# Performance work log

Measured on AMD Instinct MI355X. Metric: run time of the kernel, lower is better.

## Reference

```python
import jax, jax.numpy as jnp
import numpy as np

B, T, I, H, O = 256, 512, 64, 512, 1


def setup_inputs() -> dict:
    key = jax.random.key(0)
    ks = jax.random.split(key, 8)
    s_ih = 1.0 / np.sqrt(H)
    inp = {
        "x": jax.random.normal(ks[0], (B, T, I), dtype=jnp.float32),
        "W_ih": jax.random.uniform(ks[1], (4 * H, I), minval=-s_ih, maxval=s_ih, dtype=jnp.float32),
        "W_hh": jax.random.uniform(ks[2], (4 * H, H), minval=-s_ih, maxval=s_ih, dtype=jnp.float32),
        "b_ih": jax.random.uniform(ks[3], (4 * H,), minval=-s_ih, maxval=s_ih, dtype=jnp.float32),
        "b_hh": jax.random.uniform(ks[4], (4 * H,), minval=-s_ih, maxval=s_ih, dtype=jnp.float32),
        "W_fc": jax.random.uniform(ks[5], (O, H), minval=-s_ih, maxval=s_ih, dtype=jnp.float32),
        "b_fc": jax.random.uniform(ks[6], (O,), minval=-s_ih, maxval=s_ih, dtype=jnp.float32),
    }
    return inp


def _lstm_last_h(x, W_ih, W_hh, b_ih, b_hh):
    # x: [B, T, I]. Precompute input projection for all timesteps (one big GEMM).
    x_gates = jnp.einsum("bti,gi->btg", x, W_ih) + b_ih + b_hh  # [B, T, 4H]
    x_gates = jnp.swapaxes(x_gates, 0, 1)  # [T, B, 4H] for scan
    hdim = W_hh.shape[1]
    h0 = jnp.zeros((x.shape[0], hdim), dtype=x.dtype)
    c0 = jnp.zeros((x.shape[0], hdim), dtype=x.dtype)

    def step(carry, xg):
        h, c = carry
        gates = xg + h @ W_hh.T  # [B, 4H]
        i, f, g, o = jnp.split(gates, 4, axis=-1)  # PyTorch gate order: i, f, g, o
        i = jax.nn.sigmoid(i)
        f = jax.nn.sigmoid(f)
        g = jnp.tanh(g)
        o = jax.nn.sigmoid(o)
        c = f * c + i * g
        h = o * jnp.tanh(c)
        return (h, c), None

    (h_last, _), _ = jax.lax.scan(step, (h0, c0), x_gates)
    return h_last  # [B, H] == out[:, -1, :] for a single-layer LSTM


def reference(x, W_ih, W_hh, b_ih, b_hh, W_fc, b_fc):
    h_last = _lstm_last_h(x, W_ih, W_hh, b_ih, b_hh)
    return h_last @ W_fc.T + b_fc  # [B, O]
```

## Files before the change

### kernel.cpp

```cpp
#include <hip/hip_runtime.h>

typedef _Float16 h8 __attribute__((ext_vector_type(8)));
typedef float v4f __attribute__((ext_vector_type(4)));

#define B_  256
#define T_  512
#define I_  64
#define H_  512

#define OFF_W16   0
#define OFF_WIH   (OFF_W16 + 2048*512*2)
#define OFF_BIAS  (OFF_WIH + 2048*64*2)
#define OFF_X16   (OFF_BIAS + 2048*4)
#define OFF_H0    (OFF_X16 + 512*256*64*2)
#define OFF_H1    (OFF_H0 + 256*512*2)
#define OFF_CTR   (OFF_H1 + 256*512*2)

__device__ __forceinline__ float sigf(float x) {
    float e = __builtin_amdgcn_exp2f(-1.442695041f * x);
    return __builtin_amdgcn_rcpf(1.f + e);
}
__device__ __forceinline__ float tanhf_(float x) {
    float e = __builtin_amdgcn_exp2f(2.885390082f * x);
    return 1.f - 2.f * __builtin_amdgcn_rcpf(e + 1.f);
}

union Pack4 { _Float16 f[4]; unsigned long long u; };

__global__ void prep_w(const float* __restrict__ Wih, const float* __restrict__ Whh,
                       const float* __restrict__ bih, const float* __restrict__ bhh,
                       _Float16* __restrict__ W16, _Float16* __restrict__ Wih16,
                       float* __restrict__ bias, _Float16* __restrict__ h0,
                       unsigned* __restrict__ ctr) {
    int idx = blockIdx.x * 256 + threadIdx.x;
    W16[idx] = (_Float16)Whh[idx];
    if (idx < 2048 * 64)  Wih16[idx] = (_Float16)Wih[idx];
    if (idx < 2048)       bias[idx] = bih[idx] + bhh[idx];
    if (idx < 32768)
        __hip_atomic_store((unsigned long long*)h0 + idx, 0ull,
                           __ATOMIC_RELAXED, __HIP_MEMORY_SCOPE_AGENT);
    if (idx < 128)
        __hip_atomic_store(ctr + idx, 0u, __ATOMIC_RELAXED, __HIP_MEMORY_SCOPE_AGENT);
}

__global__ void prep_x(const float* __restrict__ x, _Float16* __restrict__ x16) {
    int idx = blockIdx.x * 256 + threadIdx.x;
    int t = idx >> 14;
    int rem = idx & 16383;
    int b = rem >> 6;
    int i = rem & 63;
    x16[idx] = (_Float16)x[((size_t)b * T_ + t) * I_ + i];
}

__launch_bounds__(256, 1)
__global__ void lstm_k(const _Float16* __restrict__ W16, const _Float16* __restrict__ Wih16,
                       const float* __restrict__ bias, const _Float16* __restrict__ x16,
                       _Float16* __restrict__ h0, _Float16* __restrict__ h1,
                       unsigned* __restrict__ ctr) {
    __shared__ _Float16 Als[18][33][40];
    __shared__ float    S[32][132];

    const int tid  = threadIdx.x;
    const int lane = tid & 63;
    const int wave = tid >> 6;
    const int bg = blockIdx.x & 7;
    const int cg = blockIdx.x >> 3;
    const int B0 = bg * 32;
    const int J0 = cg * 32;
    const int r  = lane & 15;
    const int q  = lane >> 4;

    h8 bfrag[2][18];
    float biasv[2];
#pragma unroll
    for (int t = 0; t < 2; ++t) {
        const int wrow = wave * H_ + J0 + t * 16 + r;
#pragma unroll
        for (int kk = 0; kk < 16; ++kk)
            bfrag[t][kk] = *(const h8*)(W16 + (size_t)wrow * H_ + kk * 32 + q * 8);
#pragma unroll
        for (int kk = 16; kk < 18; ++kk)
            bfrag[t][kk] = *(const h8*)(Wih16 + (size_t)wrow * I_ + (kk - 16) * 32 + q * 8);
        biasv[t] = bias[wrow];
    }

    const int er = tid >> 3;
    const int ec = (tid & 7) * 4;
    float c[4] = {0.f, 0.f, 0.f, 0.f};

    unsigned* myctr = ctr + bg * 16;

    const int xrow = tid >> 3, xs8 = tid & 7;
    h8 xv = *(const h8*)(x16 + ((size_t)B0 + xrow) * I_ + xs8 * 8);

    for (int s = 0; s < T_; ++s) {
        const _Float16* hp = (s & 1) ? h1 : h0;
        _Float16*       hn = (s & 1) ? h0 : h1;

        {
            const unsigned long long* hp64 =
                (const unsigned long long*)(hp + (size_t)B0 * H_);
            unsigned long long hv[16];
#pragma unroll
            for (int it = 0; it < 16; ++it)
                hv[it] = __hip_atomic_load(hp64 + tid + 256 * it,
                                           __ATOMIC_RELAXED, __HIP_MEMORY_SCOPE_AGENT);
            *(h8*)&Als[16 + (xs8 >> 2)][xrow][(xs8 & 3) * 8] = xv;
#pragma unroll
            for (int it = 0; it < 16; ++it) {
                int n = tid + 256 * it;
                *(unsigned long long*)&Als[(n & 127) >> 3][n >> 7][(n & 7) * 4] = hv[it];
            }
        }
        __syncthreads();

        v4f a00 = {0,0,0,0}, a01 = {0,0,0,0}, a10 = {0,0,0,0}, a11 = {0,0,0,0};
#pragma unroll
        for (int kk = 0; kk < 18; ++kk) {
            h8 am0 = *(const h8*)&Als[kk][r][q * 8];
            h8 am1 = *(const h8*)&Als[kk][16 + r][q * 8];
            a00 = __builtin_amdgcn_mfma_f32_16x16x32_f16(am0, bfrag[0][kk], a00, 0, 0, 0);
            a01 = __builtin_amdgcn_mfma_f32_16x16x32_f16(am1, bfrag[0][kk], a01, 0, 0, 0);
            a10 = __builtin_amdgcn_mfma_f32_16x16x32_f16(am0, bfrag[1][kk], a10, 0, 0, 0);
            a11 = __builtin_amdgcn_mfma_f32_16x16x32_f16(am1, bfrag[1][kk], a11, 0, 0, 0);
        }
#pragma unroll
        for (int reg = 0; reg < 4; ++reg) {
            S[q * 4 + reg][wave * 32 + r]           = a00[reg] + biasv[0];
            S[16 + q * 4 + reg][wave * 32 + r]      = a01[reg] + biasv[0];
            S[q * 4 + reg][wave * 32 + 16 + r]      = a10[reg] + biasv[1];
            S[16 + q * 4 + reg][wave * 32 + 16 + r] = a11[reg] + biasv[1];
        }
        __syncthreads();

        {
            Pack4 pk;
#pragma unroll
            for (int j = 0; j < 3 + 1; ++j) {
                float iv = sigf  (S[er][ec + j]);
                float fv = sigf  (S[er][32 + ec + j]);
                float gv = tanhf_(S[er][64 + ec + j]);
                float ov = sigf  (S[er][96 + ec + j]);
                c[j] = fv * c[j] + iv * gv;
                pk.f[j] = (_Float16)(ov * tanhf_(c[j]));
            }
            __hip_atomic_store(
                (unsigned long long*)(hn + ((size_t)B0 + er) * H_ + J0 + ec),
                pk.u, __ATOMIC_RELAXED, __HIP_MEMORY_SCOPE_AGENT);
        }
        __syncthreads();

        if (tid == 0)
            __hip_atomic_fetch_add(myctr, 1u, __ATOMIC_RELAXED, __HIP_MEMORY_SCOPE_AGENT);
        if (s + 1 < T_)
            xv = *(const h8*)(x16 + (((size_t)(s + 1)) * B_ + B0 + xrow) * I_ + xs8 * 8);
        if (tid == 0) {
            const unsigned target = 16u * (unsigned)(s + 1);
            int guard = 0;
            while (__hip_atomic_load(myctr, __ATOMIC_RELAXED, __HIP_MEMORY_SCOPE_AGENT) < target) {
                __builtin_amdgcn_s_sleep(1);
                if (++guard > (1 << 17)) break;
            }
        }
        __syncthreads();
    }
}

__global__ void fc_k(const _Float16* __restrict__ hlast, const float* __restrict__ Wfc,
                     const float* __restrict__ bfc, float* __restrict__ out) {
    int b = blockIdx.x;
    int lane = threadIdx.x;
    const unsigned long long* hp64 = (const unsigned long long*)(hlast + (size_t)b * H_);
    Pack4 p0, p1;
    p0.u = __hip_atomic_load(hp64 + lane * 2,     __ATOMIC_RELAXED, __HIP_MEMORY_SCOPE_AGENT);
    p1.u = __hip_atomic_load(hp64 + lane * 2 + 1, __ATOMIC_RELAXED, __HIP_MEMORY_SCOPE_AGENT);
    float sum = 0.f;
#pragma unroll
    for (int j = 0; j < 4; ++j) sum += (float)p0.f[j] * Wfc[lane * 8 + j];
#pragma unroll
    for (int j = 0; j < 4; ++j) sum += (float)p1.f[j] * Wfc[lane * 8 + 4 + j];
    for (int off = 32; off; off >>= 1) sum += __shfl_down(sum, off);
    if (lane == 0) out[b] = sum + bfc[0];
}

extern "C" void kernel_launch(void* const* d_in, const int* in_sizes, int n_in,
                              void* d_out, int out_size, void* d_ws, size_t ws_size,
                              hipStream_t stream) {
    (void)in_sizes; (void)n_in; (void)out_size; (void)ws_size;
    const float* x   = (const float*)d_in[0];
    const float* Wih = (const float*)d_in[1];
    const float* Whh = (const float*)d_in[2];
    const float* bih = (const float*)d_in[3];
    const float* bhh = (const float*)d_in[4];
    const float* Wfc = (const float*)d_in[5];
    const float* bfc = (const float*)d_in[6];
    float* out = (float*)d_out;

    char* ws = (char*)d_ws;
    _Float16* W16   = (_Float16*)(ws + OFF_W16);
    _Float16* Wih16 = (_Float16*)(ws + OFF_WIH);
    float*    biasf = (float*)(ws + OFF_BIAS);
    _Float16* x16   = (_Float16*)(ws + OFF_X16);
    _Float16* h0b   = (_Float16*)(ws + OFF_H0);
    _Float16* h1b   = (_Float16*)(ws + OFF_H1);
    unsigned* ctrb  = (unsigned*)(ws + OFF_CTR);

    hipLaunchKernelGGL(prep_w, dim3((2048 * 512) / 256), dim3(256), 0, stream,
                       Wih, Whh, bih, bhh, W16, Wih16, biasf, h0b, ctrb);
    hipLaunchKernelGGL(prep_x, dim3((512 * 256 * 64) / 256), dim3(256), 0, stream, x, x16);
    hipLaunchKernelGGL(lstm_k, dim3(128), dim3(256), 0, stream,
                       W16, Wih16, biasf, x16, h0b, h1b, ctrb);
    hipLaunchKernelGGL(fc_k, dim3(256), dim3(64), 0, stream, h0b, Wfc, bfc, out);
}
```

Before: 1.497 ms.

## Repartition LSTM blocks so each wave owns all four gates; use per-wave flag barrier

Blocks now cover 16 batch rows by 64 hidden units instead of 32 by 32. Each wave holds the i,f,g,o weight fragments for its own 16 hidden columns, so the gate nonlinearities and cell update run directly on the MFMA accumulators. This removes the shared-memory gate staging buffer and two block barriers per step. The atomic-add step counter is replaced by per-wave sentinel flags that each wave writes after its h stores drain, and that 32 threads poll. The h tile now sits in an XOR-swizzled LDS layout, but the h stores become scattered 2-byte atomics and bfrag register pressure doubles.

```diff
diff --git a/kernel.cpp b/kernel.cpp
--- a/kernel.cpp
+++ b/kernel.cpp
@@ -2,6 +2,7 @@
 
 typedef _Float16 h8 __attribute__((ext_vector_type(8)));
 typedef float v4f __attribute__((ext_vector_type(4)));
+typedef unsigned long long u64;
 
 #define B_  256
 #define T_  512
@@ -14,7 +15,7 @@
 #define OFF_X16   (OFF_BIAS + 2048*4)
 #define OFF_H0    (OFF_X16 + 512*256*64*2)
 #define OFF_H1    (OFF_H0 + 256*512*2)
-#define OFF_CTR   (OFF_H1 + 256*512*2)
+#define OFF_SNT   (OFF_H1 + 256*512*2)
 
 __device__ __forceinline__ float sigf(float x) {
     float e = __builtin_amdgcn_exp2f(-1.442695041f * x);
@@ -24,23 +25,21 @@
     float e = __builtin_amdgcn_exp2f(2.885390082f * x);
     return 1.f - 2.f * __builtin_amdgcn_rcpf(e + 1.f);
 }
-
-union Pack4 { _Float16 f[4]; unsigned long long u; };
 
 __global__ void prep_w(const float* __restrict__ Wih, const float* __restrict__ Whh,
                        const float* __restrict__ bih, const float* __restrict__ bhh,
                        _Float16* __restrict__ W16, _Float16* __restrict__ Wih16,
                        float* __restrict__ bias, _Float16* __restrict__ h0,
-                       unsigned* __restrict__ ctr) {
+                       unsigned* __restrict__ snt) {
     int idx = blockIdx.x * 256 + threadIdx.x;
     W16[idx] = (_Float16)Whh[idx];
     if (idx < 2048 * 64)  Wih16[idx] = (_Float16)Wih[idx];
     if (idx < 2048)       bias[idx] = bih[idx] + bhh[idx];
     if (idx < 32768)
-        __hip_atomic_store((unsigned long long*)h0 + idx, 0ull,
+        __hip_atomic_store((u64*)h0 + idx, 0ull,
                            __ATOMIC_RELAXED, __HIP_MEMORY_SCOPE_AGENT);
-    if (idx < 128)
-        __hip_atomic_store(ctr + idx, 0u, __ATOMIC_RELAXED, __HIP_MEMORY_SCOPE_AGENT);
+    if (idx < 512)
+        __hip_atomic_store(snt + idx, 0u, __ATOMIC_RELAXED, __HIP_MEMORY_SCOPE_AGENT);
 }
 
 __global__ void prep_x(const float* __restrict__ x, _Float16* __restrict__ x16) {
@@ -56,108 +55,104 @@
 __global__ void lstm_k(const _Float16* __restrict__ W16, const _Float16* __restrict__ Wih16,
                        const float* __restrict__ bias, const _Float16* __restrict__ x16,
                        _Float16* __restrict__ h0, _Float16* __restrict__ h1,
-                       unsigned* __restrict__ ctr) {
-    __shared__ _Float16 Als[18][33][40];
-    __shared__ float    S[32][132];
+                       unsigned* __restrict__ snt) {
+    __shared__ __align__(16) char A[9 * 2048];
 
     const int tid  = threadIdx.x;
     const int lane = tid & 63;
-    const int wave = tid >> 6;
-    const int bg = blockIdx.x & 7;
-    const int cg = blockIdx.x >> 3;
-    const int B0 = bg * 32;
-    const int J0 = cg * 32;
-    const int r  = lane & 15;
-    const int q  = lane >> 4;
-
-    h8 bfrag[2][18];
-    float biasv[2];
-#pragma unroll
-    for (int t = 0; t < 2; ++t) {
-        const int wrow = wave * H_ + J0 + t * 16 + r;
+    const int wv   = tid >> 6;
+    const int bg   = blockIdx.x & 15;
+    const int cg   = blockIdx.x >> 4;
+    const int B0   = bg * 16;
+    const int J0   = cg * 64;
+    const int r    = lane & 15;
+    const int q    = lane >> 4;
+
+    h8 bfrag[4][18];
+    float biasv[4];
+#pragma unroll
+    for (int g = 0; g < 4; ++g) {
+        const int wrow = g * H_ + J0 + wv * 16 + r;
 #pragma unroll
         for (int kk = 0; kk < 16; ++kk)
-            bfrag[t][kk] = *(const h8*)(W16 + (size_t)wrow * H_ + kk * 32 + q * 8);
+            bfrag[g][kk] = *(const h8*)(W16 + (size_t)wrow * H_ + kk * 32 + q * 8);
 #pragma unroll
         for (int kk = 16; kk < 18; ++kk)
-            bfrag[t][kk] = *(const h8*)(Wih16 + (size_t)wrow * I_ + (kk - 16) * 32 + q * 8);
-        biasv[t] = bias[wrow];
+            bfrag[g][kk] = *(const h8*)(Wih16 + (size_t)wrow * I_ + (kk - 16) * 32 + q * 8);
+        biasv[g] = bias[wrow];
     }
 
-    const int er = tid >> 3;
-    const int ec = (tid & 7) * 4;
-    float c[4] = {0.f, 0.f, 0.f, 0.f};
-
-    unsigned* myctr = ctr + bg * 16;
-
-    const int xrow = tid >> 3, xs8 = tid & 7;
-    h8 xv = *(const h8*)(x16 + ((size_t)B0 + xrow) * I_ + xs8 * 8);
+    const int srow = tid >> 4;
+    const int sc   = tid & 15;
+    char* const wp = A + srow * 128 + (((sc >> 1) ^ (srow & 7)) << 4) + ((sc & 1) << 3);
+    const int rbE = r * 128 + ((q ^ (r & 7)) << 4);
+    const int rbO = rbE ^ 64;
+
+    float cc[4] = {0.f, 0.f, 0.f, 0.f};
+
+    const u64* const xp = (const u64*)x16;
+    u64 xv = xp[((size_t)(B0 + srow)) * 16 + sc];
+
+    unsigned* const mysnt = snt + bg * 32;
 
     for (int s = 0; s < T_; ++s) {
         const _Float16* hp = (s & 1) ? h1 : h0;
         _Float16*       hn = (s & 1) ? h0 : h1;
 
         {
-            const unsigned long long* hp64 =
-                (const unsigned long long*)(hp + (size_t)B0 * H_);
-            unsigned long long hv[16];
-#pragma unroll
-            for (int it = 0; it < 16; ++it)
-                hv[it] = __hip_atomic_load(hp64 + tid + 256 * it,
-                                           __ATOMIC_RELAXED, __HIP_MEMORY_SCOPE_AGENT);
-            *(h8*)&Als[16 + (xs8 >> 2)][xrow][(xs8 & 3) * 8] = xv;
-#pragma unroll
-            for (int it = 0; it < 16; ++it) {
-                int n = tid + 256 * it;
-                *(unsigned long long*)&Als[(n & 127) >> 3][n >> 7][(n & 7) * 4] = hv[it];
+            const u64* hp64 = (const u64*)hp + (size_t)(B0 + srow) * 128;
+            u64 hv[8];
+#pragma unroll
+            for (int i = 0; i < 8; ++i)
+                hv[i] = __hip_atomic_load(hp64 + sc + 16 * i,
+                                          __ATOMIC_RELAXED, __HIP_MEMORY_SCOPE_AGENT);
+#pragma unroll
+            for (int i = 0; i < 8; ++i)
+                *(u64*)(wp + i * 2048) = hv[i];
+            *(u64*)(wp + 8 * 2048) = xv;
+        }
+        __syncthreads();
+
+        if (s + 1 < T_)
+            xv = xp[((size_t)(s + 1) * B_ + B0 + srow) * 16 + sc];
+
+        v4f a0 = {0,0,0,0}, a1 = {0,0,0,0}, a2 = {0,0,0,0}, a3 = {0,0,0,0};
+#pragma unroll
+        for (int kk = 0; kk < 18; ++kk) {
+            const h8 av = *(const h8*)(A + (kk >> 1) * 2048 + ((kk & 1) ? rbO : rbE));
+            a0 = __builtin_amdgcn_mfma_f32_16x16x32_f16(av, bfrag[0][kk], a0, 0, 0, 0);
+            a1 = __builtin_amdgcn_mfma_f32_16x16x32_f16(av, bfrag[1][kk], a1, 0, 0, 0);
+            a2 = __builtin_amdgcn_mfma_f32_16x16x32_f16(av, bfrag[2][kk], a2, 0, 0, 0);
+            a3 = __builtin_amdgcn_mfma_f32_16x16x32_f16(av, bfrag[3][kk], a3, 0, 0, 0);
+        }
+
+        {
+            unsigned short* hw = (unsigned short*)hn
+                               + (size_t)(B0 + q * 4) * H_ + J0 + wv * 16 + r;
+#pragma unroll
+            for (int reg = 0; reg < 4; ++reg) {
+                float iv = sigf  (a0[reg] + biasv[0]);
+                float fv = sigf  (a1[reg] + biasv[1]);
+                float gv = tanhf_(a2[reg] + biasv[2]);
+                float ov = sigf  (a3[reg] + biasv[3]);
+                cc[reg] = fv * cc[reg] + iv * gv;
+                union { _Float16 f; unsigned short u; } cv;
+                cv.f = (_Float16)(ov * tanhf_(cc[reg]));
+                __hip_atomic_store(hw + (size_t)reg * H_, cv.u,
+                                   __ATOMIC_RELAXED, __HIP_MEMORY_SCOPE_AGENT);
             }
         }
-        __syncthreads();
-
-        v4f a00 = {0,0,0,0}, a01 = {0,0,0,0}, a10 = {0,0,0,0}, a11 = {0,0,0,0};
-#pragma unroll
-        for (int kk = 0; kk < 18; ++kk) {
-            h8 am0 = *(const h8*)&Als[kk][r][q * 8];
-            h8 am1 = *(const h8*)&Als[kk][16 + r][q * 8];
-            a00 = __builtin_amdgcn_mfma_f32_16x16x32_f16(am0, bfrag[0][kk], a00, 0, 0, 0);
-            a01 = __builtin_amdgcn_mfma_f32_16x16x32_f16(am1, bfrag[0][kk], a01, 0, 0, 0);
-            a10 = __builtin_amdgcn_mfma_f32_16x16x32_f16(am0, bfrag[1][kk], a10, 0, 0, 0);
-            a11 = __builtin_amdgcn_mfma_f32_16x16x32_f16(am1, bfrag[1][kk], a11, 0, 0, 0);
-        }
-#pragma unroll
-        for (int reg = 0; reg < 4; ++reg) {
-            S[q * 4 + reg][wave * 32 + r]           = a00[reg] + biasv[0];
-            S[16 + q * 4 + reg][wave * 32 + r]      = a01[reg] + biasv[0];
-            S[q * 4 + reg][wave * 32 + 16 + r]      = a10[reg] + biasv[1];
-            S[16 + q * 4 + reg][wave * 32 + 16 + r] = a11[reg] + biasv[1];
-        }
-        __syncthreads();
-
-        {
-            Pack4 pk;
-#pragma unroll
-            for (int j = 0; j < 3 + 1; ++j) {
-                float iv = sigf  (S[er][ec + j]);
-                float fv = sigf  (S[er][32 + ec + j]);
-                float gv = tanhf_(S[er][64 + ec + j]);
-                float ov = sigf  (S[er][96 + ec + j]);
-                c[j] = fv * c[j] + iv * gv;
-                pk.f[j] = (_Float16)(ov * tanhf_(c[j]));
-            }
-            __hip_atomic_store(
-                (unsigned long long*)(hn + ((size_t)B0 + er) * H_ + J0 + ec),
-                pk.u, __ATOMIC_RELAXED, __HIP_MEMORY_SCOPE_AGENT);
-        }
-        __syncthreads();
-
-        if (tid == 0)
-            __hip_atomic_fetch_add(myctr, 1u, __ATOMIC_RELAXED, __HIP_MEMORY_SCOPE_AGENT);
-        if (s + 1 < T_)
-            xv = *(const h8*)(x16 + (((size_t)(s + 1)) * B_ + B0 + xrow) * I_ + xs8 * 8);
-        if (tid == 0) {
-            const unsigned target = 16u * (unsigned)(s + 1);
+
+        asm volatile("s_waitcnt vmcnt(0)" ::: "memory");
+        if (lane == 0)
+            __hip_atomic_store(mysnt + cg * 4 + wv, (unsigned)(s + 1),
+                               __ATOMIC_RELAXED, __HIP_MEMORY_SCOPE_AGENT);
+
+        if (tid < 32) {
+            const unsigned tgt = (unsigned)(s + 1);
             int guard = 0;
-            while (__hip_atomic_load(myctr, __ATOMIC_RELAXED, __HIP_MEMORY_SCOPE_AGENT) < target) {
+            while (__hip_atomic_load(mysnt + tid,
+                                     __ATOMIC_RELAXED, __HIP_MEMORY_SCOPE_AGENT) < tgt) {
                 __builtin_amdgcn_s_sleep(1);
                 if (++guard > (1 << 17)) break;
             }
@@ -170,8 +165,8 @@
                      const float* __restrict__ bfc, float* __restrict__ out) {
     int b = blockIdx.x;
     int lane = threadIdx.x;
-    const unsigned long long* hp64 = (const unsigned long long*)(hlast + (size_t)b * H_);
-    Pack4 p0, p1;
+    const u64* hp64 = (const u64*)(hlast + (size_t)b * H_);
+    union { _Float16 f[4]; u64 u; } p0, p1;
     p0.u = __hip_atomic_load(hp64 + lane * 2,     __ATOMIC_RELAXED, __HIP_MEMORY_SCOPE_AGENT);
     p1.u = __hip_atomic_load(hp64 + lane * 2 + 1, __ATOMIC_RELAXED, __HIP_MEMORY_SCOPE_AGENT);
     float sum = 0.f;
@@ -203,12 +198,12 @@
     _Float16* x16   = (_Float16*)(ws + OFF_X16);
     _Float16* h0b   = (_Float16*)(ws + OFF_H0);
     _Float16* h1b   = (_Float16*)(ws + OFF_H1);
-    unsigned* ctrb  = (unsigned*)(ws + OFF_CTR);
+    unsigned* sntb  = (unsigned*)(ws + OFF_SNT);
 
     hipLaunchKernelGGL(prep_w, dim3((2048 * 512) / 256), dim3(256), 0, stream,
-                       Wih, Whh, bih, bhh, W16, Wih16, biasf, h0b, ctrb);
+                       Wih, Whh, bih, bhh, W16, Wih16, biasf, h0b, sntb);
     hipLaunchKernelGGL(prep_x, dim3((512 * 256 * 64) / 256), dim3(256), 0, stream, x, x16);
     hipLaunchKernelGGL(lstm_k, dim3(128), dim3(256), 0, stream,
-                       W16, Wih16, biasf, x16, h0b, h1b, ctrb);
+                       W16, Wih16, biasf, x16, h0b, h1b, sntb);
     hipLaunchKernelGGL(fc_k, dim3(256), dim3(64), 0, stream, h0b, Wfc, bfc, out);
 }
```

Result: slower. 1.809 ms (+20.9%).

## Replace atomic counter barrier with per-wave flags and swizzle gate scratch

Applied to the files above, without the earlier changes.

The per-group atomic fetch_add counter barrier, with its single polling thread, is replaced by per-wave sentinel flags. Each wave stores its step number after draining its global stores, and every wave polls all 64 flags of its batch group with a wave-wide __all, which removes one __syncthreads and the serialized atomic RMW. The gate scratch buffer in shared memory is also given an XOR-swizzled layout so each thread reads its i/f/g/o gates as 16-byte vector loads with fewer bank conflicts. The cost is more polling traffic from all waves, and correctness now depends on relaxed stores becoming visible after the vmcnt wait.

```diff
diff --git a/kernel.cpp b/kernel.cpp
--- a/kernel.cpp
+++ b/kernel.cpp
@@ -2,6 +2,7 @@
 
 typedef _Float16 h8 __attribute__((ext_vector_type(8)));
 typedef float v4f __attribute__((ext_vector_type(4)));
+typedef unsigned long long u64;
 
 #define B_  256
 #define T_  512
@@ -14,7 +15,7 @@
 #define OFF_X16   (OFF_BIAS + 2048*4)
 #define OFF_H0    (OFF_X16 + 512*256*64*2)
 #define OFF_H1    (OFF_H0 + 256*512*2)
-#define OFF_CTR   (OFF_H1 + 256*512*2)
+#define OFF_SNT   (OFF_H1 + 256*512*2)
 
 __device__ __forceinline__ float sigf(float x) {
     float e = __builtin_amdgcn_exp2f(-1.442695041f * x);
@@ -25,22 +26,22 @@
     return 1.f - 2.f * __builtin_amdgcn_rcpf(e + 1.f);
 }
 
-union Pack4 { _Float16 f[4]; unsigned long long u; };
+union Pack4 { _Float16 f[4]; u64 u; };
 
 __global__ void prep_w(const float* __restrict__ Wih, const float* __restrict__ Whh,
                        const float* __restrict__ bih, const float* __restrict__ bhh,
                        _Float16* __restrict__ W16, _Float16* __restrict__ Wih16,
                        float* __restrict__ bias, _Float16* __restrict__ h0,
-                       unsigned* __restrict__ ctr) {
+                       unsigned* __restrict__ snt) {
     int idx = blockIdx.x * 256 + threadIdx.x;
     W16[idx] = (_Float16)Whh[idx];
     if (idx < 2048 * 64)  Wih16[idx] = (_Float16)Wih[idx];
     if (idx < 2048)       bias[idx] = bih[idx] + bhh[idx];
     if (idx < 32768)
-        __hip_atomic_store((unsigned long long*)h0 + idx, 0ull,
+        __hip_atomic_store((u64*)h0 + idx, 0ull,
                            __ATOMIC_RELAXED, __HIP_MEMORY_SCOPE_AGENT);
-    if (idx < 128)
-        __hip_atomic_store(ctr + idx, 0u, __ATOMIC_RELAXED, __HIP_MEMORY_SCOPE_AGENT);
+    if (idx < 512)
+        __hip_atomic_store(snt + idx, 0u, __ATOMIC_RELAXED, __HIP_MEMORY_SCOPE_AGENT);
 }
 
 __global__ void prep_x(const float* __restrict__ x, _Float16* __restrict__ x16) {
@@ -56,9 +57,9 @@
 __global__ void lstm_k(const _Float16* __restrict__ W16, const _Float16* __restrict__ Wih16,
                        const float* __restrict__ bias, const _Float16* __restrict__ x16,
                        _Float16* __restrict__ h0, _Float16* __restrict__ h1,
-                       unsigned* __restrict__ ctr) {
+                       unsigned* __restrict__ snt) {
     __shared__ _Float16 Als[18][33][40];
-    __shared__ float    S[32][132];
+    __shared__ __align__(16) char Sb[32 * 512];
 
     const int tid  = threadIdx.x;
     const int lane = tid & 63;
@@ -88,7 +89,18 @@
     const int ec = (tid & 7) * 4;
     float c[4] = {0.f, 0.f, 0.f, 0.f};
 
-    unsigned* myctr = ctr + bg * 16;
+    int wba[2][4];
+#pragma unroll
+    for (int t = 0; t < 2; ++t)
+#pragma unroll
+        for (int reg = 0; reg < 4; ++reg) {
+            int row = q * 4 + reg;
+            int u   = wave * 8 + t * 4 + (r >> 2);
+            wba[t][reg] = row * 512 + (((u ^ (row & 7)) << 4) | ((r & 3) << 2));
+        }
+    const int rbase = er * 512 + (((tid & 7) ^ (er & 7)) << 4);
+
+    unsigned* const mysnt = snt + bg * 64;
 
     const int xrow = tid >> 3, xs8 = tid & 7;
     h8 xv = *(const h8*)(x16 + ((size_t)B0 + xrow) * I_ + xs8 * 8);
@@ -98,9 +110,8 @@
         _Float16*       hn = (s & 1) ? h0 : h1;
 
         {
-            const unsigned long long* hp64 =
-                (const unsigned long long*)(hp + (size_t)B0 * H_);
-            unsigned long long hv[16];
+            const u64* hp64 = (const u64*)(hp + (size_t)B0 * H_);
+            u64 hv[16];
 #pragma unroll
             for (int it = 0; it < 16; ++it)
                 hv[it] = __hip_atomic_load(hp64 + tid + 256 * it,
@@ -109,7 +120,7 @@
 #pragma unroll
             for (int it = 0; it < 16; ++it) {
                 int n = tid + 256 * it;
-                *(unsigned long long*)&Als[(n & 127) >> 3][n >> 7][(n & 7) * 4] = hv[it];
+                *(u64*)&Als[(n & 127) >> 3][n >> 7][(n & 7) * 4] = hv[it];
             }
         }
         __syncthreads();
@@ -126,41 +137,49 @@
         }
 #pragma unroll
         for (int reg = 0; reg < 4; ++reg) {
-            S[q * 4 + reg][wave * 32 + r]           = a00[reg] + biasv[0];
-            S[16 + q * 4 + reg][wave * 32 + r]      = a01[reg] + biasv[0];
-            S[q * 4 + reg][wave * 32 + 16 + r]      = a10[reg] + biasv[1];
-            S[16 + q * 4 + reg][wave * 32 + 16 + r] = a11[reg] + biasv[1];
+            *(float*)(Sb + wba[0][reg])        = a00[reg] + biasv[0];
+            *(float*)(Sb + wba[0][reg] + 8192) = a01[reg] + biasv[0];
+            *(float*)(Sb + wba[1][reg])        = a10[reg] + biasv[1];
+            *(float*)(Sb + wba[1][reg] + 8192) = a11[reg] + biasv[1];
         }
         __syncthreads();
 
         {
+            v4f vi = *(const v4f*)(Sb + rbase);
+            v4f vf = *(const v4f*)(Sb + rbase + 128);
+            v4f vg = *(const v4f*)(Sb + rbase + 256);
+            v4f vo = *(const v4f*)(Sb + rbase + 384);
             Pack4 pk;
 #pragma unroll
-            for (int j = 0; j < 3 + 1; ++j) {
-                float iv = sigf  (S[er][ec + j]);
-                float fv = sigf  (S[er][32 + ec + j]);
-                float gv = tanhf_(S[er][64 + ec + j]);
-                float ov = sigf  (S[er][96 + ec + j]);
+            for (int j = 0; j < 4; ++j) {
+                float iv = sigf  (vi[j]);
+                float fv = sigf  (vf[j]);
+                float gv = tanhf_(vg[j]);
+                float ov = sigf  (vo[j]);
                 c[j] = fv * c[j] + iv * gv;
                 pk.f[j] = (_Float16)(ov * tanhf_(c[j]));
             }
             __hip_atomic_store(
-                (unsigned long long*)(hn + ((size_t)B0 + er) * H_ + J0 + ec),
+                (u64*)(hn + ((size_t)B0 + er) * H_ + J0 + ec),
                 pk.u, __ATOMIC_RELAXED, __HIP_MEMORY_SCOPE_AGENT);
         }
-        __syncthreads();
-
-        if (tid == 0)
-            __hip_atomic_fetch_add(myctr, 1u, __ATOMIC_RELAXED, __HIP_MEMORY_SCOPE_AGENT);
+
+        asm volatile("s_waitcnt vmcnt(0)" ::: "memory");
+        if (lane == 0)
+            __hip_atomic_store(mysnt + cg * 4 + wave, (unsigned)(s + 1),
+                               __ATOMIC_RELAXED, __HIP_MEMORY_SCOPE_AGENT);
         if (s + 1 < T_)
             xv = *(const h8*)(x16 + (((size_t)(s + 1)) * B_ + B0 + xrow) * I_ + xs8 * 8);
-        if (tid == 0) {
-            const unsigned target = 16u * (unsigned)(s + 1);
-            int guard = 0;
-            while (__hip_atomic_load(myctr, __ATOMIC_RELAXED, __HIP_MEMORY_SCOPE_AGENT) < target) {
-                __builtin_amdgcn_s_sleep(1);
-                if (++guard > (1 << 17)) break;
-            }
+
+        {
+            const unsigned tgt = (unsigned)(s + 1);
+            int guard = 0, done = 0;
+            do {
+                unsigned v = __hip_atomic_load(mysnt + lane,
+                                               __ATOMIC_RELAXED, __HIP_MEMORY_SCOPE_AGENT);
+                done = __all((int)(v >= tgt));
+                if (!done) __builtin_amdgcn_s_sleep(1);
+            } while (!done && ++guard < (1 << 17));
         }
         __syncthreads();
     }
@@ -170,7 +189,7 @@
                      const float* __restrict__ bfc, float* __restrict__ out) {
     int b = blockIdx.x;
     int lane = threadIdx.x;
-    const unsigned long long* hp64 = (const unsigned long long*)(hlast + (size_t)b * H_);
+    const u64* hp64 = (const u64*)(hlast + (size_t)b * H_);
     Pack4 p0, p1;
     p0.u = __hip_atomic_load(hp64 + lane * 2,     __ATOMIC_RELAXED, __HIP_MEMORY_SCOPE_AGENT);
     p1.u = __hip_atomic_load(hp64 + lane * 2 + 1, __ATOMIC_RELAXED, __HIP_MEMORY_SCOPE_AGENT);
@@ -203,12 +222,12 @@
     _Float16* x16   = (_Float16*)(ws + OFF_X16);
     _Float16* h0b   = (_Float16*)(ws + OFF_H0);
     _Float16* h1b   = (_Float16*)(ws + OFF_H1);
-    unsigned* ctrb  = (unsigned*)(ws + OFF_CTR);
+    unsigned* sntb  = (unsigned*)(ws + OFF_SNT);
 
     hipLaunchKernelGGL(prep_w, dim3((2048 * 512) / 256), dim3(256), 0, stream,
-                       Wih, Whh, bih, bhh, W16, Wih16, biasf, h0b, ctrb);
+                       Wih, Whh, bih, bhh, W16, Wih16, biasf, h0b, sntb);
     hipLaunchKernelGGL(prep_x, dim3((512 * 256 * 64) / 256), dim3(256), 0, stream, x, x16);
     hipLaunchKernelGGL(lstm_k, dim3(128), dim3(256), 0, stream,
-                       W16, Wih16, biasf, x16, h0b, h1b, ctrb);
+                       W16, Wih16, biasf, x16, h0b, h1b, sntb);
     hipLaunchKernelGGL(fc_k, dim3(256), dim3(64), 0, stream, h0b, Wfc, bfc, out);
 }
```

Result: slower. 3.063 ms (+104.6%).
